# Optimization experiments

Hardware: AMD Instinct MI355X
Metric: run time of the kernel (lower is better)

Reference implementation:

```python
import jax, jax.numpy as jnp
import numpy as np

B, S, I, H, C = 512, 512, 28, 128, 10


def setup_inputs() -> dict:
    key = jax.random.key(0)
    ks = jax.random.split(key, 11)
    std = 1.0 / np.sqrt(H)  # torch nn.RNN init scale
    u = lambda k, shape: jax.random.uniform(k, shape, jnp.float32, -std, std)
    return {
        "x": jax.random.normal(ks[0], (B, S, I), jnp.float32),
        "W_ih0": u(ks[1], (H, I)),
        "W_hh0": u(ks[2], (H, H)),
        "b_ih0": u(ks[3], (H,)),
        "b_hh0": u(ks[4], (H,)),
        "W_ih1": u(ks[5], (H, H)),
        "W_hh1": u(ks[6], (H, H)),
        "b_ih1": u(ks[7], (H,)),
        "b_hh1": u(ks[8], (H,)),
        "W_fc": u(ks[9], (C, H)),
        "b_fc": u(ks[10], (C,)),
    }


def reference(x, W_ih0, W_hh0, b_ih0, b_hh0, W_ih1, W_hh1, b_ih1, b_hh1, W_fc, b_fc):
    # 2-layer tanh RNN (batch_first); only the last timestep of layer 1 feeds fc,
    # so we carry hidden states through a scan without storing outputs.
    b = x.shape[0]
    h0_init = jnp.zeros((b, W_hh0.shape[0]), x.dtype)
    h1_init = jnp.zeros((b, W_hh1.shape[0]), x.dtype)

    def step(carry, xt):  # xt: [B, I]
        h0, h1 = carry
        h0 = jnp.tanh(xt @ W_ih0.T + b_ih0 + h0 @ W_hh0.T + b_hh0)
        h1 = jnp.tanh(h0 @ W_ih1.T + b_ih1 + h1 @ W_hh1.T + b_hh1)
        return (h0, h1), None

    xs = jnp.swapaxes(x, 0, 1)  # [S, B, I] time-major for scan
    (h0, h1), _ = jax.lax.scan(step, (h0_init, h1_init), xs)
    return h1 @ W_fc.T + b_fc  # [B, C]
```

## Files before the change

kernel.cpp:

```cpp
#include <hip/hip_runtime.h>

#define SEQ   512
#define IN    28
#define HID   128
#define NCLS  10
#define MB    16
#define PCH   144
#define MAGICF 12582912.0f

typedef __attribute__((ext_vector_type(4))) int   i32x4;
typedef __attribute__((ext_vector_type(4))) float f32x4;
typedef __attribute__((ext_vector_type(8))) short short8v;

#define SH_AA (1.0f/130048.0f)

__device__ __forceinline__ unsigned short f2bf(float f) {
    unsigned u = __float_as_uint(f);
    return (unsigned short)((u + 0x7FFFu + ((u >> 16) & 1u)) >> 16);
}
__device__ __forceinline__ float bf2f(unsigned short h) {
    return __uint_as_float(((unsigned)h) << 16);
}
__device__ __forceinline__ void split2(float f, unsigned short& hi, unsigned short& lo) {
    hi = f2bf(f);
    lo = f2bf(f - bf2f(hi));
}
__device__ __forceinline__ unsigned cvtpk(float a, float b) {
    unsigned r;
    asm("v_cvt_pk_bf16_f32 %0, %1, %2" : "=v"(r) : "v"(a), "v"(b));
    return r;
}
__device__ __forceinline__ float fast_tanh(float x) {
    float e = __expf(2.0f * x);
    return 1.0f - 2.0f * __builtin_amdgcn_rcpf(e + 1.0f);
}
__device__ __forceinline__ f32x4 mfma_bf(short8v a, short8v b, f32x4 c) {
    return __builtin_amdgcn_mfma_f32_16x16x32_bf16(a, b, c, 0, 0, 0);
}
__device__ __forceinline__ i32x4 mfma_i8(i32x4 a, i32x4 b, i32x4 c) {
    return __builtin_amdgcn_mfma_i32_16x16x64_i8(a, b, c, 0, 0, 0);
}
__device__ __forceinline__ void quantW(float wv, signed char& qa, signed char& qb) {
    int a = (int)rintf(wv * 1024.0f);
    float r = fmaf((float)a, -1.0f / 1024.0f, wv);
    int b = (int)rintf(r * 262144.0f);
    b = b > 127 ? 127 : (b < -127 ? -127 : b);
    qa = (signed char)a;
    qb = (signed char)b;
}
__device__ __forceinline__ unsigned quant4a(float t0, float t1, float t2, float t3) {
    unsigned u0 = __float_as_uint(fmaf(t0, 127.0f, MAGICF));
    unsigned u1 = __float_as_uint(fmaf(t1, 127.0f, MAGICF));
    unsigned u2 = __float_as_uint(fmaf(t2, 127.0f, MAGICF));
    unsigned u3 = __float_as_uint(fmaf(t3, 127.0f, MAGICF));
    return (u0 & 0xFFu) | ((u1 & 0xFFu) << 8) | ((u2 & 0xFFu) << 16) | ((u3 & 0xFFu) << 24);
}

union FragI8 { i32x4 v; signed char c[16]; };
union FragBF { short8v s; unsigned u[4]; };

__global__ __launch_bounds__(1024)
void rnn2_i8t(const float* __restrict__ x,
              const float* __restrict__ W_ih0, const float* __restrict__ W_hh0,
              const float* __restrict__ b_ih0, const float* __restrict__ b_hh0,
              const float* __restrict__ W_ih1, const float* __restrict__ W_hh1,
              const float* __restrict__ b_ih1, const float* __restrict__ b_hh1,
              const float* __restrict__ W_fc,  const float* __restrict__ b_fc,
              float* __restrict__ out)
{
    __shared__ __attribute__((aligned(16))) signed char hmem[2][2][MB * PCH];
    __shared__ float hfin[MB][HID + 4];

    const int t    = threadIdx.x;
    const int lane = t & 63;
    const int w    = t >> 6;
    const int lm   = lane & 15;
    const int lg   = lane >> 4;
    const int b0   = blockIdx.x * MB;
    const bool isL0 = (w < 8);
    const int T    = isL0 ? w : (w - 8);
    const int j    = 16 * T + lm;

    i32x4 Wa[2][2], Wb[2][2];
    short8v WxH = {}, WxL = {};
    float biasv[4];

    if (isL0) {
        #pragma unroll
        for (int kt = 0; kt < 2; ++kt) {
            const float* p = W_hh0 + j * HID + 64 * kt + 16 * lg;
            FragI8 a, b;
            #pragma unroll
            for (int e = 0; e < 16; ++e) quantW(p[e], a.c[e], b.c[e]);
            Wa[0][kt] = a.v; Wb[0][kt] = b.v;
        }
        FragBF H, L;
        #pragma unroll
        for (int p = 0; p < 4; ++p) {
            const int k0 = 8 * lg + 2 * p, k1 = k0 + 1;
            float w0 = (k0 < IN) ? W_ih0[j * IN + k0] : 0.0f;
            float w1 = (k1 < IN) ? W_ih0[j * IN + k1] : 0.0f;
            unsigned short h0s, l0s, h1s, l1s;
            split2(w0, h0s, l0s);
            split2(w1, h1s, l1s);
            H.u[p] = (unsigned)h0s | ((unsigned)h1s << 16);
            L.u[p] = (unsigned)l0s | ((unsigned)l1s << 16);
        }
        WxH = H.s; WxL = L.s;
        #pragma unroll
        for (int r = 0; r < 4; ++r) {
            const int u = 16 * T + 4 * lg + r;
            biasv[r] = b_ih0[u] + b_hh0[u];
        }
    } else {
        #pragma unroll
        for (int kt = 0; kt < 2; ++kt) {
            const float* p1 = W_ih1 + j * HID + 64 * kt + 16 * lg;
            const float* p2 = W_hh1 + j * HID + 64 * kt + 16 * lg;
            FragI8 a1, q1, a2, q2;
            #pragma unroll
            for (int e = 0; e < 16; ++e) {
                quantW(p1[e], a1.c[e], q1.c[e]);
                quantW(p2[e], a2.c[e], q2.c[e]);
            }
            Wa[0][kt] = a1.v; Wb[0][kt] = q1.v;
            Wa[1][kt] = a2.v; Wb[1][kt] = q2.v;
        }
        #pragma unroll
        for (int r = 0; r < 4; ++r) {
            const int u = 16 * T + 4 * lg + r;
            biasv[r] = b_ih1[u] + b_hh1[u];
        }
    }

    {
        int* z = (int*)&hmem[0][0][0];
        #pragma unroll
        for (int i = 0; i < 3; ++i) {
            const int idx = t + i * 1024;
            if (idx < (int)(sizeof(hmem) / 4)) z[idx] = 0;
        }
    }

    const float* xp = x + ((size_t)(b0 + lm) * SEQ) * IN + 8 * lg;
    float4 xA = make_float4(0.f, 0.f, 0.f, 0.f), xB = xA;
    if (isL0) {
        xA = *(const float4*)xp;
        if (lg < 3) xB = *(const float4*)(xp + 4);
    }
    __syncthreads();

    const int rbase = lm * PCH + 16 * lg;
    const int wbase = lm * PCH + 16 * T + 4 * lg;
    const i32x4 z4 = {0, 0, 0, 0};

    for (int it = 0; it <= SEQ; ++it) {
        const int rd = it & 1, wr = rd ^ 1;

        if (isL0) {
            i32x4 Ba0[2];
            Ba0[0] = *(const i32x4*)&hmem[0][rd][rbase];
            Ba0[1] = *(const i32x4*)&hmem[0][rd][rbase + 64];

            short8v BxH, BxL;
            {
                FragBF H, L;
                H.u[0] = cvtpk(xA.x, xA.y);
                H.u[1] = cvtpk(xA.z, xA.w);
                H.u[2] = cvtpk(xB.x, xB.y);
                H.u[3] = cvtpk(xB.z, xB.w);
                L.u[0] = cvtpk(xA.x - __uint_as_float(H.u[0] << 16),
                               xA.y - __uint_as_float(H.u[0] & 0xFFFF0000u));
                L.u[1] = cvtpk(xA.z - __uint_as_float(H.u[1] << 16),
                               xA.w - __uint_as_float(H.u[1] & 0xFFFF0000u));
                L.u[2] = cvtpk(xB.x - __uint_as_float(H.u[2] << 16),
                               xB.y - __uint_as_float(H.u[2] & 0xFFFF0000u));
                L.u[3] = cvtpk(xB.z - __uint_as_float(H.u[3] << 16),
                               xB.w - __uint_as_float(H.u[3] & 0xFFFF0000u));
                BxH = H.s; BxL = L.s;
            }
            {
                const int tn = (it < SEQ - 1) ? it + 1 : SEQ - 1;
                const float* p = xp + (size_t)tn * IN;
                xA = *(const float4*)p;
                xB = (lg < 3) ? *(const float4*)(p + 4) : make_float4(0.f, 0.f, 0.f, 0.f);
            }

            f32x4 accx = {biasv[0], biasv[1], biasv[2], biasv[3]};
            accx = mfma_bf(WxH, BxH, accx);
            accx = mfma_bf(WxL, BxH, accx);
            accx = mfma_bf(WxH, BxL, accx);

            i32x4 aa = mfma_i8(Wa[0][0], Ba0[0], z4);
            aa = mfma_i8(Wa[0][1], Ba0[1], aa);
            i32x4 cr = mfma_i8(Wb[0][0], Ba0[0], z4);
            cr = mfma_i8(Wb[0][1], Ba0[1], cr);

            float t0 = fast_tanh(accx[0] + SH_AA * fmaf((float)cr[0], 1.0f / 256.0f, (float)aa[0]));
            float t1 = fast_tanh(accx[1] + SH_AA * fmaf((float)cr[1], 1.0f / 256.0f, (float)aa[1]));
            float t2 = fast_tanh(accx[2] + SH_AA * fmaf((float)cr[2], 1.0f / 256.0f, (float)aa[2]));
            float t3 = fast_tanh(accx[3] + SH_AA * fmaf((float)cr[3], 1.0f / 256.0f, (float)aa[3]));
            *(unsigned*)&hmem[0][wr][wbase] = quant4a(t0, t1, t2, t3);
        } else {
            i32x4 Ba0[2], Ba1[2];
            Ba0[0] = *(const i32x4*)&hmem[0][rd][rbase];
            Ba0[1] = *(const i32x4*)&hmem[0][rd][rbase + 64];
            Ba1[0] = *(const i32x4*)&hmem[1][rd][rbase];
            Ba1[1] = *(const i32x4*)&hmem[1][rd][rbase + 64];

            i32x4 aa = mfma_i8(Wa[0][0], Ba0[0], z4);
            aa = mfma_i8(Wa[0][1], Ba0[1], aa);
            aa = mfma_i8(Wa[1][0], Ba1[0], aa);
            aa = mfma_i8(Wa[1][1], Ba1[1], aa);
            i32x4 cr = mfma_i8(Wb[0][0], Ba0[0], z4);
            cr = mfma_i8(Wb[0][1], Ba0[1], cr);
            cr = mfma_i8(Wb[1][0], Ba1[0], cr);
            cr = mfma_i8(Wb[1][1], Ba1[1], cr);

            float t0, t1, t2, t3;
            if (it == 0) {
                t0 = t1 = t2 = t3 = 0.0f;
            } else {
                t0 = fast_tanh(biasv[0] + SH_AA * fmaf((float)cr[0], 1.0f / 256.0f, (float)aa[0]));
                t1 = fast_tanh(biasv[1] + SH_AA * fmaf((float)cr[1], 1.0f / 256.0f, (float)aa[1]));
                t2 = fast_tanh(biasv[2] + SH_AA * fmaf((float)cr[2], 1.0f / 256.0f, (float)aa[2]));
                t3 = fast_tanh(biasv[3] + SH_AA * fmaf((float)cr[3], 1.0f / 256.0f, (float)aa[3]));
            }
            *(unsigned*)&hmem[1][wr][wbase] = quant4a(t0, t1, t2, t3);
            if (it == SEQ) {
                const int u = 16 * T + 4 * lg;
                hfin[lm][u + 0] = t0;
                hfin[lm][u + 1] = t1;
                hfin[lm][u + 2] = t2;
                hfin[lm][u + 3] = t3;
            }
        }
        __syncthreads();
    }

    if (t < MB * NCLS) {
        const int r = t / NCLS, c = t % NCLS;
        float acc = b_fc[c];
        const float* hf = &hfin[r][0];
        #pragma unroll 4
        for (int k = 0; k < HID; ++k)
            acc = fmaf(W_fc[c * HID + k], hf[k], acc);
        out[(b0 + r) * NCLS + c] = acc;
    }
}

extern "C" void kernel_launch(void* const* d_in, const int* in_sizes, int n_in,
                              void* d_out, int out_size, void* d_ws, size_t ws_size,
                              hipStream_t stream) {
    const float* x     = (const float*)d_in[0];
    const float* W_ih0 = (const float*)d_in[1];
    const float* W_hh0 = (const float*)d_in[2];
    const float* b_ih0 = (const float*)d_in[3];
    const float* b_hh0 = (const float*)d_in[4];
    const float* W_ih1 = (const float*)d_in[5];
    const float* W_hh1 = (const float*)d_in[6];
    const float* b_ih1 = (const float*)d_in[7];
    const float* b_hh1 = (const float*)d_in[8];
    const float* W_fc  = (const float*)d_in[9];
    const float* b_fc  = (const float*)d_in[10];
    float* out = (float*)d_out;

    rnn2_i8t<<<dim3(512 / MB), dim3(1024), 0, stream>>>(
        x, W_ih0, W_hh0, b_ih0, b_hh0, W_ih1, W_hh1, b_ih1, b_hh1, W_fc, b_fc, out);
}
```

Before: 329.4 us.

## Drop bf16 split for input projection, peel first/last steps, trim per-step ALU

The layer-0 input projection changes from three bf16 MFMAs (hi/lo split of weights and inputs) to a single bf16 MFMA, which lowers precision. The first and last timesteps are peeled out of the loop, removing the per-iteration it==0 and it==SEQ branches. tanh now uses exp2f with a folded constant, int8 packing uses v_perm, and the bias add is fused into an FMA. The LDS row pitch also changes from 144 to 160. Together these cut per-step latency on the serial recurrence, at the cost of input-projection accuracy.

```diff
diff --git a/kernel.cpp b/kernel.cpp
--- a/kernel.cpp
+++ b/kernel.cpp
@@ -5,7 +5,7 @@
 #define HID   128
 #define NCLS  10
 #define MB    16
-#define PCH   144
+#define PCH   160
 #define MAGICF 12582912.0f
 
 typedef __attribute__((ext_vector_type(4))) int   i32x4;
@@ -17,13 +17,6 @@
 __device__ __forceinline__ unsigned short f2bf(float f) {
     unsigned u = __float_as_uint(f);
     return (unsigned short)((u + 0x7FFFu + ((u >> 16) & 1u)) >> 16);
-}
-__device__ __forceinline__ float bf2f(unsigned short h) {
-    return __uint_as_float(((unsigned)h) << 16);
-}
-__device__ __forceinline__ void split2(float f, unsigned short& hi, unsigned short& lo) {
-    hi = f2bf(f);
-    lo = f2bf(f - bf2f(hi));
 }
 __device__ __forceinline__ unsigned cvtpk(float a, float b) {
     unsigned r;
@@ -31,7 +24,7 @@
     return r;
 }
 __device__ __forceinline__ float fast_tanh(float x) {
-    float e = __expf(2.0f * x);
+    float e = exp2f(x * 2.8853900817779268f);
     return 1.0f - 2.0f * __builtin_amdgcn_rcpf(e + 1.0f);
 }
 __device__ __forceinline__ f32x4 mfma_bf(short8v a, short8v b, f32x4 c) {
@@ -53,14 +46,16 @@
     unsigned u1 = __float_as_uint(fmaf(t1, 127.0f, MAGICF));
     unsigned u2 = __float_as_uint(fmaf(t2, 127.0f, MAGICF));
     unsigned u3 = __float_as_uint(fmaf(t3, 127.0f, MAGICF));
-    return (u0 & 0xFFu) | ((u1 & 0xFFu) << 8) | ((u2 & 0xFFu) << 16) | ((u3 & 0xFFu) << 24);
+    unsigned t01 = __builtin_amdgcn_perm(u1, u0, 0x00000400u);
+    unsigned t23 = __builtin_amdgcn_perm(u3, u2, 0x00000400u);
+    return __builtin_amdgcn_perm(t23, t01, 0x05040100u);
 }
 
 union FragI8 { i32x4 v; signed char c[16]; };
 union FragBF { short8v s; unsigned u[4]; };
 
 __global__ __launch_bounds__(1024)
-void rnn2_i8t(const float* __restrict__ x,
+void rnn2_i8u(const float* __restrict__ x,
               const float* __restrict__ W_ih0, const float* __restrict__ W_hh0,
               const float* __restrict__ b_ih0, const float* __restrict__ b_hh0,
               const float* __restrict__ W_ih1, const float* __restrict__ W_hh1,
@@ -82,7 +77,7 @@
     const int j    = 16 * T + lm;
 
     i32x4 Wa[2][2], Wb[2][2];
-    short8v WxH = {}, WxL = {};
+    short8v WxH = {};
     float biasv[4];
 
     if (isL0) {
@@ -94,19 +89,15 @@
             for (int e = 0; e < 16; ++e) quantW(p[e], a.c[e], b.c[e]);
             Wa[0][kt] = a.v; Wb[0][kt] = b.v;
         }
-        FragBF H, L;
+        FragBF H;
         #pragma unroll
         for (int p = 0; p < 4; ++p) {
             const int k0 = 8 * lg + 2 * p, k1 = k0 + 1;
             float w0 = (k0 < IN) ? W_ih0[j * IN + k0] : 0.0f;
             float w1 = (k1 < IN) ? W_ih0[j * IN + k1] : 0.0f;
-            unsigned short h0s, l0s, h1s, l1s;
-            split2(w0, h0s, l0s);
-            split2(w1, h1s, l1s);
-            H.u[p] = (unsigned)h0s | ((unsigned)h1s << 16);
-            L.u[p] = (unsigned)l0s | ((unsigned)l1s << 16);
-        }
-        WxH = H.s; WxL = L.s;
+            H.u[p] = (unsigned)f2bf(w0) | ((unsigned)f2bf(w1) << 16);
+        }
+        WxH = H.s;
         #pragma unroll
         for (int r = 0; r < 4; ++r) {
             const int u = 16 * T + 4 * lg + r;
@@ -154,7 +145,25 @@
     const int wbase = lm * PCH + 16 * T + 4 * lg;
     const i32x4 z4 = {0, 0, 0, 0};
 
-    for (int it = 0; it <= SEQ; ++it) {
+    if (isL0) {
+        FragBF H;
+        H.u[0] = cvtpk(xA.x, xA.y);
+        H.u[1] = cvtpk(xA.z, xA.w);
+        H.u[2] = cvtpk(xB.x, xB.y);
+        H.u[3] = cvtpk(xB.z, xB.w);
+        {
+            const float* p = xp + IN;
+            xA = *(const float4*)p;
+            xB = (lg < 3) ? *(const float4*)(p + 4) : make_float4(0.f, 0.f, 0.f, 0.f);
+        }
+        f32x4 accx = {biasv[0], biasv[1], biasv[2], biasv[3]};
+        accx = mfma_bf(WxH, H.s, accx);
+        *(unsigned*)&hmem[0][1][wbase] = quant4a(fast_tanh(accx[0]), fast_tanh(accx[1]),
+                                                 fast_tanh(accx[2]), fast_tanh(accx[3]));
+    }
+    __syncthreads();
+
+    for (int it = 1; it < SEQ; ++it) {
         const int rd = it & 1, wr = rd ^ 1;
 
         if (isL0) {
@@ -162,44 +171,30 @@
             Ba0[0] = *(const i32x4*)&hmem[0][rd][rbase];
             Ba0[1] = *(const i32x4*)&hmem[0][rd][rbase + 64];
 
-            short8v BxH, BxL;
+            FragBF H;
+            H.u[0] = cvtpk(xA.x, xA.y);
+            H.u[1] = cvtpk(xA.z, xA.w);
+            H.u[2] = cvtpk(xB.x, xB.y);
+            H.u[3] = cvtpk(xB.z, xB.w);
             {
-                FragBF H, L;
-                H.u[0] = cvtpk(xA.x, xA.y);
-                H.u[1] = cvtpk(xA.z, xA.w);
-                H.u[2] = cvtpk(xB.x, xB.y);
-                H.u[3] = cvtpk(xB.z, xB.w);
-                L.u[0] = cvtpk(xA.x - __uint_as_float(H.u[0] << 16),
-                               xA.y - __uint_as_float(H.u[0] & 0xFFFF0000u));
-                L.u[1] = cvtpk(xA.z - __uint_as_float(H.u[1] << 16),
-                               xA.w - __uint_as_float(H.u[1] & 0xFFFF0000u));
-                L.u[2] = cvtpk(xB.x - __uint_as_float(H.u[2] << 16),
-                               xB.y - __uint_as_float(H.u[2] & 0xFFFF0000u));
-                L.u[3] = cvtpk(xB.z - __uint_as_float(H.u[3] << 16),
-                               xB.w - __uint_as_float(H.u[3] & 0xFFFF0000u));
-                BxH = H.s; BxL = L.s;
-            }
-            {
-                const int tn = (it < SEQ - 1) ? it + 1 : SEQ - 1;
+                const int tn = (it < SEQ - 1) ? it + 1 : it;
                 const float* p = xp + (size_t)tn * IN;
                 xA = *(const float4*)p;
                 xB = (lg < 3) ? *(const float4*)(p + 4) : make_float4(0.f, 0.f, 0.f, 0.f);
             }
 
             f32x4 accx = {biasv[0], biasv[1], biasv[2], biasv[3]};
-            accx = mfma_bf(WxH, BxH, accx);
-            accx = mfma_bf(WxL, BxH, accx);
-            accx = mfma_bf(WxH, BxL, accx);
+            accx = mfma_bf(WxH, H.s, accx);
 
             i32x4 aa = mfma_i8(Wa[0][0], Ba0[0], z4);
             aa = mfma_i8(Wa[0][1], Ba0[1], aa);
             i32x4 cr = mfma_i8(Wb[0][0], Ba0[0], z4);
             cr = mfma_i8(Wb[0][1], Ba0[1], cr);
 
-            float t0 = fast_tanh(accx[0] + SH_AA * fmaf((float)cr[0], 1.0f / 256.0f, (float)aa[0]));
-            float t1 = fast_tanh(accx[1] + SH_AA * fmaf((float)cr[1], 1.0f / 256.0f, (float)aa[1]));
-            float t2 = fast_tanh(accx[2] + SH_AA * fmaf((float)cr[2], 1.0f / 256.0f, (float)aa[2]));
-            float t3 = fast_tanh(accx[3] + SH_AA * fmaf((float)cr[3], 1.0f / 256.0f, (float)aa[3]));
+            float t0 = fast_tanh(fmaf(SH_AA, fmaf((float)cr[0], 1.0f / 256.0f, (float)aa[0]), accx[0]));
+            float t1 = fast_tanh(fmaf(SH_AA, fmaf((float)cr[1], 1.0f / 256.0f, (float)aa[1]), accx[1]));
+            float t2 = fast_tanh(fmaf(SH_AA, fmaf((float)cr[2], 1.0f / 256.0f, (float)aa[2]), accx[2]));
+            float t3 = fast_tanh(fmaf(SH_AA, fmaf((float)cr[3], 1.0f / 256.0f, (float)aa[3]), accx[3]));
             *(unsigned*)&hmem[0][wr][wbase] = quant4a(t0, t1, t2, t3);
         } else {
             i32x4 Ba0[2], Ba1[2];
@@ -217,26 +212,38 @@
             cr = mfma_i8(Wb[1][0], Ba1[0], cr);
             cr = mfma_i8(Wb[1][1], Ba1[1], cr);
 
-            float t0, t1, t2, t3;
-            if (it == 0) {
-                t0 = t1 = t2 = t3 = 0.0f;
-            } else {
-                t0 = fast_tanh(biasv[0] + SH_AA * fmaf((float)cr[0], 1.0f / 256.0f, (float)aa[0]));
-                t1 = fast_tanh(biasv[1] + SH_AA * fmaf((float)cr[1], 1.0f / 256.0f, (float)aa[1]));
-                t2 = fast_tanh(biasv[2] + SH_AA * fmaf((float)cr[2], 1.0f / 256.0f, (float)aa[2]));
-                t3 = fast_tanh(biasv[3] + SH_AA * fmaf((float)cr[3], 1.0f / 256.0f, (float)aa[3]));
-            }
+            float t0 = fast_tanh(fmaf(SH_AA, fmaf((float)cr[0], 1.0f / 256.0f, (float)aa[0]), biasv[0]));
+            float t1 = fast_tanh(fmaf(SH_AA, fmaf((float)cr[1], 1.0f / 256.0f, (float)aa[1]), biasv[1]));
+            float t2 = fast_tanh(fmaf(SH_AA, fmaf((float)cr[2], 1.0f / 256.0f, (float)aa[2]), biasv[2]));
+            float t3 = fast_tanh(fmaf(SH_AA, fmaf((float)cr[3], 1.0f / 256.0f, (float)aa[3]), biasv[3]));
             *(unsigned*)&hmem[1][wr][wbase] = quant4a(t0, t1, t2, t3);
-            if (it == SEQ) {
-                const int u = 16 * T + 4 * lg;
-                hfin[lm][u + 0] = t0;
-                hfin[lm][u + 1] = t1;
-                hfin[lm][u + 2] = t2;
-                hfin[lm][u + 3] = t3;
-            }
         }
         __syncthreads();
     }
+
+    if (!isL0) {
+        i32x4 Ba0[2], Ba1[2];
+        Ba0[0] = *(const i32x4*)&hmem[0][0][rbase];
+        Ba0[1] = *(const i32x4*)&hmem[0][0][rbase + 64];
+        Ba1[0] = *(const i32x4*)&hmem[1][0][rbase];
+        Ba1[1] = *(const i32x4*)&hmem[1][0][rbase + 64];
+
+        i32x4 aa = mfma_i8(Wa[0][0], Ba0[0], z4);
+        aa = mfma_i8(Wa[0][1], Ba0[1], aa);
+        aa = mfma_i8(Wa[1][0], Ba1[0], aa);
+        aa = mfma_i8(Wa[1][1], Ba1[1], aa);
+        i32x4 cr = mfma_i8(Wb[0][0], Ba0[0], z4);
+        cr = mfma_i8(Wb[0][1], Ba0[1], cr);
+        cr = mfma_i8(Wb[1][0], Ba1[0], cr);
+        cr = mfma_i8(Wb[1][1], Ba1[1], cr);
+
+        const int u = 16 * T + 4 * lg;
+        hfin[lm][u + 0] = fast_tanh(fmaf(SH_AA, fmaf((float)cr[0], 1.0f / 256.0f, (float)aa[0]), biasv[0]));
+        hfin[lm][u + 1] = fast_tanh(fmaf(SH_AA, fmaf((float)cr[1], 1.0f / 256.0f, (float)aa[1]), biasv[1]));
+        hfin[lm][u + 2] = fast_tanh(fmaf(SH_AA, fmaf((float)cr[2], 1.0f / 256.0f, (float)aa[2]), biasv[2]));
+        hfin[lm][u + 3] = fast_tanh(fmaf(SH_AA, fmaf((float)cr[3], 1.0f / 256.0f, (float)aa[3]), biasv[3]));
+    }
+    __syncthreads();
 
     if (t < MB * NCLS) {
         const int r = t / NCLS, c = t % NCLS;
@@ -265,6 +272,6 @@
     const float* b_fc  = (const float*)d_in[10];
     float* out = (float*)d_out;
 
-    rnn2_i8t<<<dim3(512 / MB), dim3(1024), 0, stream>>>(
+    rnn2_i8u<<<dim3(512 / MB), dim3(1024), 0, stream>>>(
         x, W_ih0, W_hh0, b_ih0, b_hh0, W_ih1, W_hh1, b_ih1, b_hh1, W_fc, b_fc, out);
 }
```

Result: slower. 353.2 us (+7.2%).
